# Kernel tuning notes

Measured on AMD Instinct MI355X. Metric: run time of the kernel, lower is better.

The kernel has to match this reference:

```python
import jax, jax.numpy as jnp
import numpy as np

T, B = 256, 256
IN_H, IN_T, IN_R = 64, 64, 32
H1, H2, H3 = 512, 1024, 256
H = H1 + H2 + H3
IN = IN_H + IN_T + IN_R
DT, TAU = 10.0, 30.0
ALPHA = DT / TAU
SIG1, SIG2, SIG3 = 0.1, 0.1, 0.1  # sigma_rec3 = sigma_rec1
RECUR1 = RECUR2 = FFWD = FBACK = 1.0


def _readin_mask():
    m = np.zeros((H, IN), dtype=np.float32)
    # row block 1 (h1): heading + targcolor
    m[:H1, :IN_H] = 1.0
    m[:H1, IN_H:IN_H + IN_T] = 1.0
    # row block 2 (h2): rules only
    m[H1:H1 + H2, IN_H + IN_T:] = 1.0
    # row block 3 (h3): targcolor only
    m[H1 + H2:, IN_H:IN_H + IN_T] = 1.0
    return jnp.asarray(m)


def _rec_mask():
    m = np.zeros((H, H), dtype=np.float32)
    m[:H1, :H1] = RECUR1
    m[:H1, H1:H1 + H2] = FBACK
    m[H1:H1 + H2, :H1] = FFWD
    m[H1:H1 + H2, H1:H1 + H2] = RECUR2
    m[H1:H1 + H2, H1 + H2:] = 1.0
    m[H1 + H2:, H1:H1 + H2] = 1.0
    m[H1 + H2:, H1 + H2:] = 1.0
    return jnp.asarray(m)


def _sigma_vec():
    # Faithful to source bug: segment 2 covers cols [H1:H2), leaving [H2:H1+H2) noiseless.
    s = np.zeros((H,), dtype=np.float32)
    s[:H1] = SIG1
    s[H1:H2] = SIG2
    s[H1 + H2:] = SIG3
    return jnp.asarray(s)


def setup_inputs() -> dict:
    key = jax.random.key(0)
    ks = jax.random.split(key, 5)
    bnd_in = 1.0 / np.sqrt(IN)
    bnd_rec = 1.0 / np.sqrt(H)
    return {
        "inputs": jax.random.normal(ks[0], (T, B, IN), dtype=jnp.float32),
        "W_in": jax.random.uniform(ks[1], (H, IN), minval=-bnd_in, maxval=bnd_in, dtype=jnp.float32),
        "b_in": jax.random.uniform(ks[2], (H,), minval=-bnd_in, maxval=bnd_in, dtype=jnp.float32),
        "W_rec": jax.random.uniform(ks[3], (H, H), minval=-bnd_rec, maxval=bnd_rec, dtype=jnp.float32),
        "b_rec": jax.random.uniform(ks[4], (H,), minval=-bnd_rec, maxval=bnd_rec, dtype=jnp.float32),
    }


def reference(inputs, W_in, b_in, W_rec, b_rec):
    mask_in = _readin_mask()
    mask_rec = _rec_mask()
    sigma = _sigma_vec()
    Weff_in = W_in * mask_in    # [H, IN]
    Weff_rec = W_rec * mask_rec  # [H, H]

    noise_keys = jax.random.split(jax.random.key(42), T)
    # precompute input projection for all steps: [T, B, H]
    xin = jnp.einsum('tbi,hi->tbh', inputs, Weff_in) + b_in

    def step(carry, xs):
        state, out = carry
        x_t, nk = xs
        total = x_t + out @ Weff_rec.T + b_rec  # [B, H]
        state = state * (1.0 - ALPHA) + total * ALPHA
        state = state + sigma * jax.random.normal(nk, state.shape, dtype=state.dtype)
        out = jax.nn.relu(state)
        return (state, out), out

    init = (jnp.zeros((B, H), dtype=inputs.dtype), jnp.zeros((B, H), dtype=inputs.dtype))
    (state, out), outputs = jax.lax.scan(step, init, (xin, noise_keys))
    return outputs, (state, out)
```

## Files before the change

kernel.cpp:

```cpp
#include <hip/hip_runtime.h>

#define T_STEPS 256
#define B_SZ 256
#define H_SZ 1792
#define IN_SZ 160
#define BH (B_SZ * H_SZ)
#define NSTEP_REC 56
#define NSTEP_X 5
#define NFRAG_H 112
#define APK_HALF (16 * NSTEP_REC * 2 * 512)
#define KS 8

typedef __attribute__((ext_vector_type(8))) _Float16 f16x8;
typedef __attribute__((ext_vector_type(4))) _Float16 f16x4;
typedef __attribute__((ext_vector_type(4))) float f32x4;

__device__ __forceinline__ unsigned rotl32(unsigned x, int r) {
  return (x << r) | (x >> (32 - r));
}

__device__ __forceinline__ void threefry2x32(unsigned k0, unsigned k1,
                                             unsigned x0, unsigned x1,
                                             unsigned& o0, unsigned& o1) {
  unsigned ks2 = k0 ^ k1 ^ 0x1BD11BDAu;
  x0 += k0; x1 += k1;
#define TF_R(r) { x0 += x1; x1 = rotl32(x1, (r)); x1 ^= x0; }
  TF_R(13) TF_R(15) TF_R(26) TF_R(6)
  x0 += k1; x1 += ks2 + 1u;
  TF_R(17) TF_R(29) TF_R(16) TF_R(24)
  x0 += ks2; x1 += k0 + 2u;
  TF_R(13) TF_R(15) TF_R(26) TF_R(6)
  x0 += k0; x1 += k1 + 3u;
  TF_R(17) TF_R(29) TF_R(16) TF_R(24)
  x0 += k1; x1 += ks2 + 4u;
  TF_R(13) TF_R(15) TF_R(26) TF_R(6)
  x0 += ks2; x1 += k0 + 5u;
#undef TF_R
  o0 = x0; o1 = x1;
}

__device__ __forceinline__ float erfinv_f32(float x) {
  float w = -log1pf(-x * x);
  float p;
  if (w < 5.0f) {
    w -= 2.5f;
    p = 2.81022636e-08f;
    p = fmaf(p, w, 3.43273939e-07f);
    p = fmaf(p, w, -3.5233877e-06f);
    p = fmaf(p, w, -4.39150654e-06f);
    p = fmaf(p, w, 0.00021858087f);
    p = fmaf(p, w, -0.00125372503f);
    p = fmaf(p, w, -0.00417768164f);
    p = fmaf(p, w, 0.246640727f);
    p = fmaf(p, w, 1.50140941f);
  } else {
    w = sqrtf(w) - 3.0f;
    p = -0.000200214257f;
    p = fmaf(p, w, 0.000100950558f);
    p = fmaf(p, w, 0.00134934322f);
    p = fmaf(p, w, -0.00367342844f);
    p = fmaf(p, w, 0.00573950773f);
    p = fmaf(p, w, -0.0076224613f);
    p = fmaf(p, w, 0.00943887047f);
    p = fmaf(p, w, 1.00167406f);
    p = fmaf(p, w, 2.83297682f);
  }
  return p * x;
}

__device__ __forceinline__ float jax_normal(unsigned k0, unsigned k1, unsigned e) {
  unsigned o0, o1;
  threefry2x32(k0, k1, 0u, e, o0, o1);
  const unsigned bits = o0 ^ o1;
  float u = __uint_as_float((bits >> 9) | 0x3F800000u) - 1.0f;
  float z = u * 2.0f + (-0.99999994f);
  z = fmaxf(-0.99999994f, z);
  return 1.4142135623730951f * erfinv_f32(z);
}

__global__ void init_keys_kernel(unsigned* __restrict__ keybuf) {
  const unsigned t = threadIdx.x;
  unsigned o0, o1;
  threefry2x32(0u, 42u, 0u, t, o0, o1);
  keybuf[2 * t] = o0;
  keybuf[2 * t + 1] = o1;
}

__device__ __forceinline__ void split2(float w, _Float16& h, _Float16& m) {
  h = (_Float16)w;
  float r = w - (float)h;
  m = (_Float16)(r * 2048.0f);
}

__global__ void pack_B_kernel(const float* __restrict__ W_in,
                              const float* __restrict__ W_rec,
                              _Float16* __restrict__ Bpk) {
  const int id = blockIdx.x * 256 + threadIdx.x;
  const int h = id / 244;
  const int ko = id - h * 244;
  const int k0 = ko * 8;
  float w[8];
  if (k0 < H_SZ) {
    const float4* src = reinterpret_cast<const float4*>(&W_rec[(size_t)h * H_SZ + k0]);
    float4 v0 = src[0], v1 = src[1];
    float m;
    if (h < 512)       m = (k0 < 1536) ? 1.0f : 0.0f;
    else if (h < 1536) m = 1.0f;
    else               m = (k0 >= 512) ? 1.0f : 0.0f;
    w[0]=v0.x*m; w[1]=v0.y*m; w[2]=v0.z*m; w[3]=v0.w*m;
    w[4]=v1.x*m; w[5]=v1.y*m; w[6]=v1.z*m; w[7]=v1.w*m;
  } else {
    const int i0 = k0 - H_SZ;
    const float4* src = reinterpret_cast<const float4*>(&W_in[(size_t)h * IN_SZ + i0]);
    float4 v0 = src[0], v1 = src[1];
    float m;
    if (h < 512)       m = (i0 < 128) ? 1.0f : 0.0f;
    else if (h < 1536) m = (i0 >= 128) ? 1.0f : 0.0f;
    else               m = (i0 >= 64 && i0 < 128) ? 1.0f : 0.0f;
    w[0]=v0.x*m; w[1]=v0.y*m; w[2]=v0.z*m; w[3]=v0.w*m;
    w[4]=v1.x*m; w[5]=v1.y*m; w[6]=v1.z*m; w[7]=v1.w*m;
  }
  f16x8 vh, vm;
#pragma unroll
  for (int j = 0; j < 8; ++j) {
    _Float16 a, b;
    split2(w[j], a, b);
    vh[j] = a; vm[j] = b;
  }
  const int s = ko >> 2;
  const int f = h >> 4;
  const int lane = (h & 15) + 16 * (ko & 3);
  _Float16* dst = Bpk + ((size_t)(s * NFRAG_H + f) * 2) * 512 + lane * 8;
  *reinterpret_cast<f16x8*>(dst)       = vh;
  *reinterpret_cast<f16x8*>(dst + 512) = vm;
}

__global__ void pack_x_kernel(const float* __restrict__ inputs,
                              _Float16* __restrict__ Xpk) {
  const int id = blockIdx.x * 256 + threadIdx.x;
  const int io = id % 20;
  const int tb = id / 20;
  const int b = tb & 255;
  const int t = tb >> 8;
  const float4* src = reinterpret_cast<const float4*>(
      &inputs[((size_t)(t * 256 + b)) * IN_SZ + io * 8]);
  float4 v0 = src[0], v1 = src[1];
  float w[8] = {v0.x, v0.y, v0.z, v0.w, v1.x, v1.y, v1.z, v1.w};
  f16x8 vh, vm;
#pragma unroll
  for (int j = 0; j < 8; ++j) {
    _Float16 a, bb;
    split2(w[j], a, bb);
    vh[j] = a; vm[j] = bb;
  }
  const int sx = io >> 2;
  const int lane = (b & 15) + 16 * (io & 3);
  _Float16* dst = Xpk +
      ((size_t)((t * 16 + (b >> 4)) * NSTEP_X + sx) * 2) * 512 + lane * 8;
  *reinterpret_cast<f16x8*>(dst)       = vh;
  *reinterpret_cast<f16x8*>(dst + 512) = vm;
}

__global__ void zero_kernel(float* __restrict__ p, int n) {
  const int i = blockIdx.x * 256 + threadIdx.x;
  if (i < n) p[i] = 0.0f;
}

__global__ __launch_bounds__(256) void xin_gemm(
    const _Float16* __restrict__ Xpk,
    const _Float16* __restrict__ Bpk,
    const float* __restrict__ b_in,
    float* __restrict__ out) {
  const int tid = threadIdx.x;
  const int w = tid >> 6;
  const int lane = tid & 63;
  const int t = blockIdx.x / 28;
  const int hb = blockIdx.x - t * 28;
  const int bf0 = w * 4;
  const int f0 = hb * 4;
  const int lofs = lane * 8;

  f32x4 acc1[4][4] = {};
  f32x4 acc2[4][4] = {};
#pragma unroll
  for (int s = 0; s < NSTEP_X; ++s) {
    f16x8 a[4][2], b[4][2];
#pragma unroll
    for (int pi = 0; pi < 4; ++pi) {
      const _Float16* ap = Xpk +
          ((size_t)((t * 16 + bf0 + pi) * NSTEP_X + s) * 2) * 512 + lofs;
      a[pi][0] = *reinterpret_cast<const f16x8*>(ap);
      a[pi][1] = *reinterpret_cast<const f16x8*>(ap + 512);
    }
#pragma unroll
    for (int qi = 0; qi < 4; ++qi) {
      const _Float16* bp = Bpk +
          ((size_t)(((NSTEP_REC + s) * NFRAG_H + f0 + qi) * 2)) * 512 + lofs;
      b[qi][0] = *reinterpret_cast<const f16x8*>(bp);
      b[qi][1] = *reinterpret_cast<const f16x8*>(bp + 512);
    }
#pragma unroll
    for (int pi = 0; pi < 4; ++pi)
#pragma unroll
      for (int qi = 0; qi < 4; ++qi) {
        acc1[pi][qi] = __builtin_amdgcn_mfma_f32_16x16x32_f16(
            a[pi][0], b[qi][0], acc1[pi][qi], 0, 0, 0);
        acc2[pi][qi] = __builtin_amdgcn_mfma_f32_16x16x32_f16(
            a[pi][0], b[qi][1], acc2[pi][qi], 0, 0, 0);
        acc2[pi][qi] = __builtin_amdgcn_mfma_f32_16x16x32_f16(
            a[pi][1], b[qi][0], acc2[pi][qi], 0, 0, 0);
      }
  }
#pragma unroll
  for (int qi = 0; qi < 4; ++qi) {
    const int h = hb * 64 + qi * 16 + (lane & 15);
    const float bi = b_in[h];
#pragma unroll
    for (int pi = 0; pi < 4; ++pi) {
      const int brow = (bf0 + pi) * 16 + ((lane >> 4) << 2);
#pragma unroll
      for (int r = 0; r < 4; ++r) {
        out[(size_t)t * BH + (size_t)(brow + r) * H_SZ + h] =
            acc1[pi][qi][r] + acc2[pi][qi][r] * (1.0f / 2048.0f) + bi;
      }
    }
  }
}

__global__ __launch_bounds__(512) void eirnn_step(
    const _Float16* __restrict__ Apk_cur,
    _Float16* __restrict__ Apk_next,
    const _Float16* __restrict__ Bpk,
    float* __restrict__ state,
    const float* __restrict__ b_rec,
    const unsigned* __restrict__ keybuf,
    float* __restrict__ out_t, int t) {
  __shared__ float ldsC[KS][32][68];

  const int tid = threadIdx.x;
  const int w = tid >> 6;
  const int lane = tid & 63;
  const int logical = (blockIdx.x & 7) * 28 + (blockIdx.x >> 3);
  const int hb = logical >> 3;
  const int bb = logical & 7;
  const int b0 = bb * 32;

  const int bf0 = b0 >> 4;
  const int f0 = hb * 4;
  const int lofs = lane * 8;

  int rec_lo, n;
  if (hb < 8)       { rec_lo = 0;  n = 48; }
  else if (hb < 24) { rec_lo = 0;  n = 56; }
  else              { rec_lo = 16; n = 40; }

  f32x4 acc1[2][4] = {};
  f32x4 acc2[2][4] = {};
  f16x8 bA[2][2][2];
  f16x8 bB[2][4][2];

#define LOAD(IB, I)                                                            \
  { const int s = rec_lo + (I);                                                \
    _Pragma("unroll")                                                          \
    for (int pi = 0; pi < 2; ++pi) {                                           \
      const _Float16* ap =                                                     \
          Apk_cur + ((size_t)((bf0 + pi) * NSTEP_REC + s) * 2) * 512 + lofs;   \
      bA[IB][pi][0] = *reinterpret_cast<const f16x8*>(ap);                     \
      bA[IB][pi][1] = *reinterpret_cast<const f16x8*>(ap + 512);               \
    }                                                                          \
    _Pragma("unroll")                                                          \
    for (int qi = 0; qi < 4; ++qi) {                                           \
      const _Float16* bp =                                                     \
          Bpk + ((size_t)(s * NFRAG_H + f0 + qi) * 2) * 512 + lofs;            \
      bB[IB][qi][0] = *reinterpret_cast<const f16x8*>(bp);                     \
      bB[IB][qi][1] = *reinterpret_cast<const f16x8*>(bp + 512);               \
    } }

#define MM(IB)                                                                 \
  { _Pragma("unroll")                                                          \
    for (int pi = 0; pi < 2; ++pi)                                             \
      _Pragma("unroll")                                                        \
      for (int qi = 0; qi < 4; ++qi) {                                         \
        acc1[pi][qi] = __builtin_amdgcn_mfma_f32_16x16x32_f16(                 \
            bA[IB][pi][0], bB[IB][qi][0], acc1[pi][qi], 0, 0, 0);              \
        acc2[pi][qi] = __builtin_amdgcn_mfma_f32_16x16x32_f16(                 \
            bA[IB][pi][0], bB[IB][qi][1], acc2[pi][qi], 0, 0, 0);              \
        acc2[pi][qi] = __builtin_amdgcn_mfma_f32_16x16x32_f16(                 \
            bA[IB][pi][1], bB[IB][qi][0], acc2[pi][qi], 0, 0, 0);              \
      } }

  LOAD(0, w)
  if (w + KS < n) LOAD(1, w + KS)

  const int bl = tid >> 4;
  const int q  = tid & 15;
  const int h0 = hb * 64 + q * 4;
  const size_t e0 = (size_t)(b0 + bl) * H_SZ + h0;
  const float sig = (h0 < 1024 || h0 >= 1536) ? 0.1f : 0.0f;
  float nz[4] = {0.0f, 0.0f, 0.0f, 0.0f};
  if (sig != 0.0f) {
    const unsigned kk0 = keybuf[2 * t], kk1 = keybuf[2 * t + 1];
#pragma unroll
    for (int j = 0; j < 4; ++j)
      nz[j] = jax_normal(kk0, kk1, (unsigned)(e0 + j));
  }
  const f32x4 xi = *reinterpret_cast<const f32x4*>(&out_t[e0]);
  const f32x4 sv = *reinterpret_cast<const f32x4*>(&state[e0]);
  const f32x4 br = *reinterpret_cast<const f32x4*>(&b_rec[h0]);

  for (int i = w; i < n; i += 2 * KS) {
    MM(0)
    if (i + 2 * KS < n) LOAD(0, i + 2 * KS)
    if (i + KS < n) {
      MM(1)
      if (i + 3 * KS < n) LOAD(1, i + 3 * KS)
    }
  }
#undef LOAD
#undef MM

#pragma unroll
  for (int pi = 0; pi < 2; ++pi)
#pragma unroll
    for (int qi = 0; qi < 4; ++qi) {
      const int row = pi * 16 + ((lane >> 4) << 2);
      const int col = qi * 16 + (lane & 15);
#pragma unroll
      for (int r = 0; r < 4; ++r)
        ldsC[w][row + r][col] =
            acc1[pi][qi][r] + acc2[pi][qi][r] * (1.0f / 2048.0f);
    }
  __syncthreads();

  f32x4 sum = {0.0f, 0.0f, 0.0f, 0.0f};
#pragma unroll
  for (int ww = 0; ww < KS; ++ww)
    sum += *reinterpret_cast<const f32x4*>(&ldsC[ww][bl][q * 4]);

  f32x4 so, oo;
  f16x4 vh, vm;
#pragma unroll
  for (int j = 0; j < 4; ++j) {
    float s = sv[j] * 0.6666666865348816f +
              (sum[j] + xi[j] + br[j]) * 0.3333333432674408f;
    s += sig * nz[j];
    const float o = fmaxf(s, 0.0f);
    so[j] = s; oo[j] = o;
    _Float16 xh, xm;
    split2(o, xh, xm);
    vh[j] = xh; vm[j] = xm;
  }
  *reinterpret_cast<f32x4*>(&state[e0]) = so;
  *reinterpret_cast<f32x4*>(&out_t[e0]) = oo;

  const int b = b0 + bl;
  _Float16* dst = Apk_next +
      ((size_t)((b >> 4) * NSTEP_REC + hb * 2 + (q >> 3)) * 2) * 512 +
      ((b & 15) + 16 * ((q >> 1) & 3)) * 8 + (q & 1) * 4;
  *reinterpret_cast<f16x4*>(dst)       = vh;
  *reinterpret_cast<f16x4*>(dst + 512) = vm;
}

__global__ void finalize_kernel(const float* __restrict__ state,
                                const float* __restrict__ last_out,
                                float* __restrict__ dst) {
  const int i = blockIdx.x * 256 + threadIdx.x;
  dst[i] = state[i];
  dst[BH + i] = last_out[i];
}

extern "C" void kernel_launch(void* const* d_in, const int* in_sizes, int n_in,
                              void* d_out, int out_size, void* d_ws, size_t ws_size,
                              hipStream_t stream) {
  const float* inputs = (const float*)d_in[0];
  const float* W_in   = (const float*)d_in[1];
  const float* b_in   = (const float*)d_in[2];
  const float* W_rec  = (const float*)d_in[3];
  const float* b_rec  = (const float*)d_in[4];
  float* out = (float*)d_out;

  char* ws = (char*)d_ws;
  _Float16* Bpk = (_Float16*)ws;
  _Float16* Xpk = (_Float16*)(ws + 13991936);
  _Float16* Apk = (_Float16*)(ws + 55934976);
  float* state  = (float*)(ws + 59604992);
  unsigned* keybuf = (unsigned*)(ws + 61440000);

  init_keys_kernel<<<1, 256, 0, stream>>>(keybuf);
  pack_B_kernel<<<1708, 256, 0, stream>>>(W_in, W_rec, Bpk);
  pack_x_kernel<<<5120, 256, 0, stream>>>(inputs, Xpk);
  zero_kernel<<<1792, 256, 0, stream>>>(state, BH);
  zero_kernel<<<1792, 256, 0, stream>>>((float*)Apk, APK_HALF / 2);

  xin_gemm<<<T_STEPS * 28, 256, 0, stream>>>(Xpk, Bpk, b_in, out);

  for (int t = 0; t < T_STEPS; ++t) {
    const int par = t & 1;
    eirnn_step<<<224, 512, 0, stream>>>(
        Apk + (size_t)par * APK_HALF,
        Apk + (size_t)(par ^ 1) * APK_HALF,
        Bpk, state, b_rec, keybuf, out + (size_t)t * BH, t);
  }

  finalize_kernel<<<1792, 256, 0, stream>>>(
      state, out + (size_t)(T_STEPS - 1) * BH, out + (size_t)T_STEPS * BH);
}
```

Baseline: 3.380 ms.

## Replace per-step RNN launches with persistent kernel and software grid barrier

Merges the 256 per-timestep launches into one persistent kernel of 224 blocks. The blocks synchronise through an atomic generation-counter grid barrier. State stays in registers across steps. The previous step's fp32 output is read directly from the output buffer and split into fp16 hi/lo in registers, which removes the packed Apk buffers, the zero kernels and the finalize kernel. This cuts launch overhead and some global traffic, in exchange for a spin barrier that relies on all blocks being co-resident, plus extra conversion work and wider fp32 A loads inside the MFMA loop.

Result: slower. 6.618 ms (+95.8%).

```diff
diff --git a/kernel.cpp b/kernel.cpp
--- a/kernel.cpp
+++ b/kernel.cpp
@@ -8,12 +8,14 @@
 #define NSTEP_REC 56
 #define NSTEP_X 5
 #define NFRAG_H 112
-#define APK_HALF (16 * NSTEP_REC * 2 * 512)
 #define KS 8
+#define NBLOCKS 224
 
 typedef __attribute__((ext_vector_type(8))) _Float16 f16x8;
-typedef __attribute__((ext_vector_type(4))) _Float16 f16x4;
 typedef __attribute__((ext_vector_type(4))) float f32x4;
+typedef unsigned long long u64;
+
+union U64F32x4 { u64 u[2]; f32x4 v; };
 
 __device__ __forceinline__ unsigned rotl32(unsigned x, int r) {
   return (x << r) | (x >> (32 - r));
@@ -78,12 +80,14 @@
   return 1.4142135623730951f * erfinv_f32(z);
 }
 
-__global__ void init_keys_kernel(unsigned* __restrict__ keybuf) {
+__global__ void init_keys_kernel(unsigned* __restrict__ keybuf,
+                                 unsigned* __restrict__ bar) {
   const unsigned t = threadIdx.x;
   unsigned o0, o1;
   threefry2x32(0u, 42u, 0u, t, o0, o1);
   keybuf[2 * t] = o0;
   keybuf[2 * t + 1] = o1;
+  if (t == 0) bar[0] = 0u;
 }
 
 __device__ __forceinline__ void split2(float w, _Float16& h, _Float16& m) {
@@ -161,11 +165,6 @@
   *reinterpret_cast<f16x8*>(dst + 512) = vm;
 }
 
-__global__ void zero_kernel(float* __restrict__ p, int n) {
-  const int i = blockIdx.x * 256 + threadIdx.x;
-  if (i < n) p[i] = 0.0f;
-}
-
 __global__ __launch_bounds__(256) void xin_gemm(
     const _Float16* __restrict__ Xpk,
     const _Float16* __restrict__ Bpk,
@@ -227,14 +226,33 @@
   }
 }
 
-__global__ __launch_bounds__(512) void eirnn_step(
-    const _Float16* __restrict__ Apk_cur,
-    _Float16* __restrict__ Apk_next,
+__device__ __forceinline__ void grid_barrier(unsigned* bar) {
+  __syncthreads();
+  if (threadIdx.x == 0) {
+    const unsigned gen = __hip_atomic_load(bar + 1, __ATOMIC_RELAXED,
+                                           __HIP_MEMORY_SCOPE_AGENT);
+    const unsigned pos = __hip_atomic_fetch_add(bar, 1u, __ATOMIC_RELAXED,
+                                                __HIP_MEMORY_SCOPE_AGENT);
+    if (pos == NBLOCKS - 1) {
+      __hip_atomic_store(bar, 0u, __ATOMIC_RELAXED, __HIP_MEMORY_SCOPE_AGENT);
+      __hip_atomic_store(bar + 1, gen + 1u, __ATOMIC_RELAXED,
+                         __HIP_MEMORY_SCOPE_AGENT);
+    } else {
+      while (__hip_atomic_load(bar + 1, __ATOMIC_RELAXED,
+                               __HIP_MEMORY_SCOPE_AGENT) == gen) {
+        __builtin_amdgcn_s_sleep(2);
+      }
+    }
+  }
+  asm volatile("" ::: "memory");
+  __syncthreads();
+}
+
+__global__ __launch_bounds__(512, 2) void eirnn_persist(
     const _Float16* __restrict__ Bpk,
-    float* __restrict__ state,
     const float* __restrict__ b_rec,
     const unsigned* __restrict__ keybuf,
-    float* __restrict__ out_t, int t) {
+    float* __restrict__ out, unsigned* __restrict__ bar) {
   __shared__ float ldsC[KS][32][68];
 
   const int tid = threadIdx.x;
@@ -245,7 +263,6 @@
   const int bb = logical & 7;
   const int b0 = bb * 32;
 
-  const int bf0 = b0 >> 4;
   const int f0 = hb * 4;
   const int lofs = lane * 8;
 
@@ -254,119 +271,143 @@
   else if (hb < 24) { rec_lo = 0;  n = 56; }
   else              { rec_lo = 16; n = 40; }
 
-  f32x4 acc1[2][4] = {};
-  f32x4 acc2[2][4] = {};
-  f16x8 bA[2][2][2];
-  f16x8 bB[2][4][2];
-
-#define LOAD(IB, I)                                                            \
-  { const int s = rec_lo + (I);                                                \
-    _Pragma("unroll")                                                          \
-    for (int pi = 0; pi < 2; ++pi) {                                           \
-      const _Float16* ap =                                                     \
-          Apk_cur + ((size_t)((bf0 + pi) * NSTEP_REC + s) * 2) * 512 + lofs;   \
-      bA[IB][pi][0] = *reinterpret_cast<const f16x8*>(ap);                     \
-      bA[IB][pi][1] = *reinterpret_cast<const f16x8*>(ap + 512);               \
-    }                                                                          \
-    _Pragma("unroll")                                                          \
-    for (int qi = 0; qi < 4; ++qi) {                                           \
-      const _Float16* bp =                                                     \
-          Bpk + ((size_t)(s * NFRAG_H + f0 + qi) * 2) * 512 + lofs;            \
-      bB[IB][qi][0] = *reinterpret_cast<const f16x8*>(bp);                     \
-      bB[IB][qi][1] = *reinterpret_cast<const f16x8*>(bp + 512);               \
-    } }
-
-#define MM(IB)                                                                 \
-  { _Pragma("unroll")                                                          \
-    for (int pi = 0; pi < 2; ++pi)                                             \
-      _Pragma("unroll")                                                        \
-      for (int qi = 0; qi < 4; ++qi) {                                         \
-        acc1[pi][qi] = __builtin_amdgcn_mfma_f32_16x16x32_f16(                 \
-            bA[IB][pi][0], bB[IB][qi][0], acc1[pi][qi], 0, 0, 0);              \
-        acc2[pi][qi] = __builtin_amdgcn_mfma_f32_16x16x32_f16(                 \
-            bA[IB][pi][0], bB[IB][qi][1], acc2[pi][qi], 0, 0, 0);              \
-        acc2[pi][qi] = __builtin_amdgcn_mfma_f32_16x16x32_f16(                 \
-            bA[IB][pi][1], bB[IB][qi][0], acc2[pi][qi], 0, 0, 0);              \
-      } }
-
-  LOAD(0, w)
-  if (w + KS < n) LOAD(1, w + KS)
+  const size_t rowbase0 =
+      (size_t)(b0 + (lane & 15)) * H_SZ + ((lane >> 4) << 3);
+  const size_t rowbase1 = rowbase0 + (size_t)16 * H_SZ;
 
   const int bl = tid >> 4;
   const int q  = tid & 15;
   const int h0 = hb * 64 + q * 4;
   const size_t e0 = (size_t)(b0 + bl) * H_SZ + h0;
   const float sig = (h0 < 1024 || h0 >= 1536) ? 0.1f : 0.0f;
-  float nz[4] = {0.0f, 0.0f, 0.0f, 0.0f};
-  if (sig != 0.0f) {
+  const f32x4 br = *reinterpret_cast<const f32x4*>(&b_rec[h0]);
+
+  f32x4 sv = {0.0f, 0.0f, 0.0f, 0.0f};
+
+#define COMPUTE_NZ_XI                                                          \
+  if (sig != 0.0f) {                                                           \
+    _Pragma("unroll")                                                          \
+    for (int j = 0; j < 4; ++j) nz[j] = jax_normal(kk0, kk1, (unsigned)(e0 + j)); \
+  }                                                                            \
+  { U64F32x4 xu;                                                               \
+    const u64* xp = (const u64*)(out + (size_t)t * BH + e0);                   \
+    xu.u[0] = __hip_atomic_load(xp, __ATOMIC_RELAXED, __HIP_MEMORY_SCOPE_AGENT); \
+    xu.u[1] = __hip_atomic_load(xp + 1, __ATOMIC_RELAXED, __HIP_MEMORY_SCOPE_AGENT); \
+    xi = xu.v; }
+
+  for (int t = 0; t < T_STEPS; ++t) {
     const unsigned kk0 = keybuf[2 * t], kk1 = keybuf[2 * t + 1];
-#pragma unroll
-    for (int j = 0; j < 4; ++j)
-      nz[j] = jax_normal(kk0, kk1, (unsigned)(e0 + j));
-  }
-  const f32x4 xi = *reinterpret_cast<const f32x4*>(&out_t[e0]);
-  const f32x4 sv = *reinterpret_cast<const f32x4*>(&state[e0]);
-  const f32x4 br = *reinterpret_cast<const f32x4*>(&b_rec[h0]);
-
-  for (int i = w; i < n; i += 2 * KS) {
-    MM(0)
-    if (i + 2 * KS < n) LOAD(0, i + 2 * KS)
-    if (i + KS < n) {
-      MM(1)
-      if (i + 3 * KS < n) LOAD(1, i + 3 * KS)
-    }
-  }
-#undef LOAD
+    float nz[4] = {0.0f, 0.0f, 0.0f, 0.0f};
+    f32x4 xi;
+    f32x4 sum = {0.0f, 0.0f, 0.0f, 0.0f};
+
+    if (t > 0) {
+      const float* outPrev = out + (size_t)(t - 1) * BH;
+      f32x4 acc1[2][4] = {};
+      f32x4 acc2[2][4] = {};
+      f32x4 rA[2][2][2];
+      f16x8 bB[2][4][2];
+
+#define LOADA(IB, I)                                                           \
+  { const int s_ = rec_lo + (I);                                               \
+    rA[IB][0][0] = *reinterpret_cast<const f32x4*>(outPrev + rowbase0 + 32 * s_);     \
+    rA[IB][0][1] = *reinterpret_cast<const f32x4*>(outPrev + rowbase0 + 32 * s_ + 4); \
+    rA[IB][1][0] = *reinterpret_cast<const f32x4*>(outPrev + rowbase1 + 32 * s_);     \
+    rA[IB][1][1] = *reinterpret_cast<const f32x4*>(outPrev + rowbase1 + 32 * s_ + 4); }
+#define LOADB(IB, I)                                                           \
+  { const int s_ = rec_lo + (I);                                               \
+    _Pragma("unroll")                                                          \
+    for (int qi = 0; qi < 4; ++qi) {                                           \
+      const _Float16* bp =                                                     \
+          Bpk + ((size_t)(s_ * NFRAG_H + f0 + qi) * 2) * 512 + lofs;           \
+      bB[IB][qi][0] = *reinterpret_cast<const f16x8*>(bp);                     \
+      bB[IB][qi][1] = *reinterpret_cast<const f16x8*>(bp + 512);               \
+    } }
+#define MM(IB)                                                                 \
+  { _Pragma("unroll")                                                          \
+    for (int pi = 0; pi < 2; ++pi) {                                           \
+      f16x8 ah, am;                                                            \
+      _Pragma("unroll")                                                        \
+      for (int c = 0; c < 2; ++c)                                              \
+        _Pragma("unroll")                                                      \
+        for (int j = 0; j < 4; ++j) {                                          \
+          const float v = rA[IB][pi][c][j];                                    \
+          const _Float16 hh = (_Float16)v;                                     \
+          const float r_ = v - (float)hh;                                      \
+          ah[c * 4 + j] = hh;                                                  \
+          am[c * 4 + j] = (_Float16)(r_ * 2048.0f);                            \
+        }                                                                      \
+      _Pragma("unroll")                                                        \
+      for (int qi = 0; qi < 4; ++qi) {                                         \
+        acc1[pi][qi] = __builtin_amdgcn_mfma_f32_16x16x32_f16(                 \
+            ah, bB[IB][qi][0], acc1[pi][qi], 0, 0, 0);                         \
+        acc2[pi][qi] = __builtin_amdgcn_mfma_f32_16x16x32_f16(                 \
+            ah, bB[IB][qi][1], acc2[pi][qi], 0, 0, 0);                         \
+        acc2[pi][qi] = __builtin_amdgcn_mfma_f32_16x16x32_f16(                 \
+            am, bB[IB][qi][0], acc2[pi][qi], 0, 0, 0);                         \
+      } } }
+
+      LOADA(0, w) LOADB(0, w)
+      if (w + KS < n) { LOADA(1, w + KS) LOADB(1, w + KS) }
+
+      COMPUTE_NZ_XI
+
+      for (int i = w; i < n; i += 2 * KS) {
+        MM(0)
+        if (i + 2 * KS < n) { LOADA(0, i + 2 * KS) LOADB(0, i + 2 * KS) }
+        if (i + KS < n) {
+          MM(1)
+          if (i + 3 * KS < n) { LOADA(1, i + 3 * KS) LOADB(1, i + 3 * KS) }
+        }
+      }
+#undef LOADA
+#undef LOADB
 #undef MM
 
 #pragma unroll
-  for (int pi = 0; pi < 2; ++pi)
-#pragma unroll
-    for (int qi = 0; qi < 4; ++qi) {
-      const int row = pi * 16 + ((lane >> 4) << 2);
-      const int col = qi * 16 + (lane & 15);
-#pragma unroll
-      for (int r = 0; r < 4; ++r)
-        ldsC[w][row + r][col] =
-            acc1[pi][qi][r] + acc2[pi][qi][r] * (1.0f / 2048.0f);
-    }
-  __syncthreads();
-
-  f32x4 sum = {0.0f, 0.0f, 0.0f, 0.0f};
-#pragma unroll
-  for (int ww = 0; ww < KS; ++ww)
-    sum += *reinterpret_cast<const f32x4*>(&ldsC[ww][bl][q * 4]);
-
-  f32x4 so, oo;
-  f16x4 vh, vm;
-#pragma unroll
-  for (int j = 0; j < 4; ++j) {
-    float s = sv[j] * 0.6666666865348816f +
-              (sum[j] + xi[j] + br[j]) * 0.3333333432674408f;
-    s += sig * nz[j];
-    const float o = fmaxf(s, 0.0f);
-    so[j] = s; oo[j] = o;
-    _Float16 xh, xm;
-    split2(o, xh, xm);
-    vh[j] = xh; vm[j] = xm;
-  }
-  *reinterpret_cast<f32x4*>(&state[e0]) = so;
-  *reinterpret_cast<f32x4*>(&out_t[e0]) = oo;
-
-  const int b = b0 + bl;
-  _Float16* dst = Apk_next +
-      ((size_t)((b >> 4) * NSTEP_REC + hb * 2 + (q >> 3)) * 2) * 512 +
-      ((b & 15) + 16 * ((q >> 1) & 3)) * 8 + (q & 1) * 4;
-  *reinterpret_cast<f16x4*>(dst)       = vh;
-  *reinterpret_cast<f16x4*>(dst + 512) = vm;
-}
-
-__global__ void finalize_kernel(const float* __restrict__ state,
-                                const float* __restrict__ last_out,
-                                float* __restrict__ dst) {
-  const int i = blockIdx.x * 256 + threadIdx.x;
-  dst[i] = state[i];
-  dst[BH + i] = last_out[i];
+      for (int pi = 0; pi < 2; ++pi)
+#pragma unroll
+        for (int qi = 0; qi < 4; ++qi) {
+          const int row = pi * 16 + ((lane >> 4) << 2);
+          const int col = qi * 16 + (lane & 15);
+#pragma unroll
+          for (int r = 0; r < 4; ++r)
+            ldsC[w][row + r][col] =
+                acc1[pi][qi][r] + acc2[pi][qi][r] * (1.0f / 2048.0f);
+        }
+      __syncthreads();
+
+#pragma unroll
+      for (int ww = 0; ww < KS; ++ww)
+        sum += *reinterpret_cast<const f32x4*>(&ldsC[ww][bl][q * 4]);
+    } else {
+      COMPUTE_NZ_XI
+    }
+
+    f32x4 so, oo;
+#pragma unroll
+    for (int j = 0; j < 4; ++j) {
+      float s = sv[j] * 0.6666666865348816f +
+                (sum[j] + xi[j] + br[j]) * 0.3333333432674408f;
+      s += sig * nz[j];
+      so[j] = s;
+      oo[j] = fmaxf(s, 0.0f);
+    }
+    sv = so;
+
+    if (t < T_STEPS - 1) {
+      U64F32x4 ou; ou.v = oo;
+      u64* op = (u64*)(out + (size_t)t * BH + e0);
+      __hip_atomic_store(op, ou.u[0], __ATOMIC_RELAXED, __HIP_MEMORY_SCOPE_AGENT);
+      __hip_atomic_store(op + 1, ou.u[1], __ATOMIC_RELAXED, __HIP_MEMORY_SCOPE_AGENT);
+      grid_barrier(bar);
+    } else {
+      *reinterpret_cast<f32x4*>(&out[(size_t)t * BH + e0]) = oo;
+      *reinterpret_cast<f32x4*>(&out[(size_t)T_STEPS * BH + e0]) = so;
+      *reinterpret_cast<f32x4*>(&out[(size_t)T_STEPS * BH + BH + e0]) = oo;
+    }
+  }
+#undef COMPUTE_NZ_XI
 }
 
 extern "C" void kernel_launch(void* const* d_in, const int* in_sizes, int n_in,
@@ -382,26 +423,14 @@
   char* ws = (char*)d_ws;
   _Float16* Bpk = (_Float16*)ws;
   _Float16* Xpk = (_Float16*)(ws + 13991936);
-  _Float16* Apk = (_Float16*)(ws + 55934976);
-  float* state  = (float*)(ws + 59604992);
-  unsigned* keybuf = (unsigned*)(ws + 61440000);
-
-  init_keys_kernel<<<1, 256, 0, stream>>>(keybuf);
+  unsigned* keybuf = (unsigned*)(ws + 55934976);
+  unsigned* bar = (unsigned*)(ws + 55937152);
+
+  init_keys_kernel<<<1, 256, 0, stream>>>(keybuf, bar);
   pack_B_kernel<<<1708, 256, 0, stream>>>(W_in, W_rec, Bpk);
   pack_x_kernel<<<5120, 256, 0, stream>>>(inputs, Xpk);
-  zero_kernel<<<1792, 256, 0, stream>>>(state, BH);
-  zero_kernel<<<1792, 256, 0, stream>>>((float*)Apk, APK_HALF / 2);
 
   xin_gemm<<<T_STEPS * 28, 256, 0, stream>>>(Xpk, Bpk, b_in, out);
 
-  for (int t = 0; t < T_STEPS; ++t) {
-    const int par = t & 1;
-    eirnn_step<<<224, 512, 0, stream>>>(
-        Apk + (size_t)par * APK_HALF,
-        Apk + (size_t)(par ^ 1) * APK_HALF,
-        Bpk, state, b_rec, keybuf, out + (size_t)t * BH, t);
-  }
-
-  finalize_kernel<<<1792, 256, 0, stream>>>(
-      state, out + (size_t)(T_STEPS - 1) * BH, out + (size_t)T_STEPS * BH);
-}
+  eirnn_persist<<<NBLOCKS, 512, 0, stream>>>(Bpk, b_rec, keybuf, out, bar);
+}
```

## Deepen recurrent step prefetch pipeline and skip zero-state first step

Applied to the files above, without the earlier changes.

The recurrent step kernel's K loop is fully unrolled into at most seven stages. A-fragments are now prefetched four stages ahead and B-fragments three ahead, replacing the old two-deep double buffer, so more global loads are in flight while MFMAs run. At t=0 the matmul is skipped because the previous output is zero, and the state is taken as zero. This removes the two zero-fill kernels for state and the packed activation buffer. It costs more registers per thread, which may lower occupancy or cause spills.

Result: slower. 4.344 ms (+28.5%).

```diff
diff --git a/kernel.cpp b/kernel.cpp
--- a/kernel.cpp
+++ b/kernel.cpp
@@ -161,11 +161,6 @@
   *reinterpret_cast<f16x8*>(dst + 512) = vm;
 }
 
-__global__ void zero_kernel(float* __restrict__ p, int n) {
-  const int i = blockIdx.x * 256 + threadIdx.x;
-  if (i < n) p[i] = 0.0f;
-}
-
 __global__ __launch_bounds__(256) void xin_gemm(
     const _Float16* __restrict__ Xpk,
     const _Float16* __restrict__ Bpk,
@@ -253,96 +248,114 @@
   if (hb < 8)       { rec_lo = 0;  n = 48; }
   else if (hb < 24) { rec_lo = 0;  n = 56; }
   else              { rec_lo = 16; n = 40; }
-
-  f32x4 acc1[2][4] = {};
-  f32x4 acc2[2][4] = {};
-  f16x8 bA[2][2][2];
-  f16x8 bB[2][4][2];
-
-#define LOAD(IB, I)                                                            \
-  { const int s = rec_lo + (I);                                                \
+  const int m = n >> 3;
+
+  const int bl = tid >> 4;
+  const int q  = tid & 15;
+  const int h0 = hb * 64 + q * 4;
+  const size_t e0 = (size_t)(b0 + bl) * H_SZ + h0;
+  const float sig = (h0 < 1024 || h0 >= 1536) ? 0.1f : 0.0f;
+
+  f32x4 sum = {0.0f, 0.0f, 0.0f, 0.0f};
+  float nz[4] = {0.0f, 0.0f, 0.0f, 0.0f};
+  f32x4 xi, sv, brv;
+
+  if (t > 0) {
+    f32x4 acc1[2][4] = {};
+    f32x4 acc2[2][4] = {};
+    f16x8 bA[4][2][2];
+    f16x8 bB[3][4][2];
+
+#define LOADA(IA, J)                                                           \
+  { const int s_ = rec_lo + w + 8 * (J);                                       \
     _Pragma("unroll")                                                          \
     for (int pi = 0; pi < 2; ++pi) {                                           \
       const _Float16* ap =                                                     \
-          Apk_cur + ((size_t)((bf0 + pi) * NSTEP_REC + s) * 2) * 512 + lofs;   \
-      bA[IB][pi][0] = *reinterpret_cast<const f16x8*>(ap);                     \
-      bA[IB][pi][1] = *reinterpret_cast<const f16x8*>(ap + 512);               \
-    }                                                                          \
+          Apk_cur + ((size_t)((bf0 + pi) * NSTEP_REC + s_) * 2) * 512 + lofs;  \
+      bA[IA][pi][0] = *reinterpret_cast<const f16x8*>(ap);                     \
+      bA[IA][pi][1] = *reinterpret_cast<const f16x8*>(ap + 512);               \
+    } }
+#define LOADB(IB, J)                                                           \
+  { const int s_ = rec_lo + w + 8 * (J);                                       \
     _Pragma("unroll")                                                          \
     for (int qi = 0; qi < 4; ++qi) {                                           \
       const _Float16* bp =                                                     \
-          Bpk + ((size_t)(s * NFRAG_H + f0 + qi) * 2) * 512 + lofs;            \
+          Bpk + ((size_t)(s_ * NFRAG_H + f0 + qi) * 2) * 512 + lofs;           \
       bB[IB][qi][0] = *reinterpret_cast<const f16x8*>(bp);                     \
       bB[IB][qi][1] = *reinterpret_cast<const f16x8*>(bp + 512);               \
     } }
-
-#define MM(IB)                                                                 \
+#define MM(IB, IA)                                                             \
   { _Pragma("unroll")                                                          \
     for (int pi = 0; pi < 2; ++pi)                                             \
       _Pragma("unroll")                                                        \
       for (int qi = 0; qi < 4; ++qi) {                                         \
         acc1[pi][qi] = __builtin_amdgcn_mfma_f32_16x16x32_f16(                 \
-            bA[IB][pi][0], bB[IB][qi][0], acc1[pi][qi], 0, 0, 0);              \
+            bA[IA][pi][0], bB[IB][qi][0], acc1[pi][qi], 0, 0, 0);              \
         acc2[pi][qi] = __builtin_amdgcn_mfma_f32_16x16x32_f16(                 \
-            bA[IB][pi][0], bB[IB][qi][1], acc2[pi][qi], 0, 0, 0);              \
+            bA[IA][pi][0], bB[IB][qi][1], acc2[pi][qi], 0, 0, 0);              \
         acc2[pi][qi] = __builtin_amdgcn_mfma_f32_16x16x32_f16(                 \
-            bA[IB][pi][1], bB[IB][qi][0], acc2[pi][qi], 0, 0, 0);              \
+            bA[IA][pi][1], bB[IB][qi][0], acc2[pi][qi], 0, 0, 0);              \
       } }
-
-  LOAD(0, w)
-  if (w + KS < n) LOAD(1, w + KS)
-
-  const int bl = tid >> 4;
-  const int q  = tid & 15;
-  const int h0 = hb * 64 + q * 4;
-  const size_t e0 = (size_t)(b0 + bl) * H_SZ + h0;
-  const float sig = (h0 < 1024 || h0 >= 1536) ? 0.1f : 0.0f;
-  float nz[4] = {0.0f, 0.0f, 0.0f, 0.0f};
-  if (sig != 0.0f) {
-    const unsigned kk0 = keybuf[2 * t], kk1 = keybuf[2 * t + 1];
-#pragma unroll
-    for (int j = 0; j < 4; ++j)
-      nz[j] = jax_normal(kk0, kk1, (unsigned)(e0 + j));
-  }
-  const f32x4 xi = *reinterpret_cast<const f32x4*>(&out_t[e0]);
-  const f32x4 sv = *reinterpret_cast<const f32x4*>(&state[e0]);
-  const f32x4 br = *reinterpret_cast<const f32x4*>(&b_rec[h0]);
-
-  for (int i = w; i < n; i += 2 * KS) {
-    MM(0)
-    if (i + 2 * KS < n) LOAD(0, i + 2 * KS)
-    if (i + KS < n) {
-      MM(1)
-      if (i + 3 * KS < n) LOAD(1, i + 3 * KS)
+#define STEP(J)                                                                \
+  if ((J) < m) {                                                               \
+    MM((J) % 3, (J) & 3)                                                       \
+    if ((J) + 3 < m) LOADB(((J) + 3) % 3, (J) + 3)                             \
+    if ((J) + 4 < m) LOADA(((J) + 4) & 3, (J) + 4)                             \
+  }
+
+    LOADA(0, 0) LOADA(1, 1) LOADA(2, 2) LOADA(3, 3)
+    LOADB(0, 0) LOADB(1, 1) LOADB(2, 2)
+
+    if (sig != 0.0f) {
+      const unsigned kk0 = keybuf[2 * t], kk1 = keybuf[2 * t + 1];
+#pragma unroll
+      for (int j = 0; j < 4; ++j)
+        nz[j] = jax_normal(kk0, kk1, (unsigned)(e0 + j));
     }
-  }
-#undef LOAD
+    xi = *reinterpret_cast<const f32x4*>(&out_t[e0]);
+    sv = *reinterpret_cast<const f32x4*>(&state[e0]);
+    brv = *reinterpret_cast<const f32x4*>(&b_rec[h0]);
+
+    STEP(0) STEP(1) STEP(2) STEP(3) STEP(4) STEP(5) STEP(6)
+#undef LOADA
+#undef LOADB
 #undef MM
-
-#pragma unroll
-  for (int pi = 0; pi < 2; ++pi)
-#pragma unroll
-    for (int qi = 0; qi < 4; ++qi) {
-      const int row = pi * 16 + ((lane >> 4) << 2);
-      const int col = qi * 16 + (lane & 15);
-#pragma unroll
-      for (int r = 0; r < 4; ++r)
-        ldsC[w][row + r][col] =
-            acc1[pi][qi][r] + acc2[pi][qi][r] * (1.0f / 2048.0f);
+#undef STEP
+
+#pragma unroll
+    for (int pi = 0; pi < 2; ++pi)
+#pragma unroll
+      for (int qi = 0; qi < 4; ++qi) {
+        const int row = pi * 16 + ((lane >> 4) << 2);
+        const int col = qi * 16 + (lane & 15);
+#pragma unroll
+        for (int r = 0; r < 4; ++r)
+          ldsC[w][row + r][col] =
+              acc1[pi][qi][r] + acc2[pi][qi][r] * (1.0f / 2048.0f);
+      }
+    __syncthreads();
+
+#pragma unroll
+    for (int ww = 0; ww < KS; ++ww)
+      sum += *reinterpret_cast<const f32x4*>(&ldsC[ww][bl][q * 4]);
+  } else {
+    if (sig != 0.0f) {
+      const unsigned kk0 = keybuf[0], kk1 = keybuf[1];
+#pragma unroll
+      for (int j = 0; j < 4; ++j)
+        nz[j] = jax_normal(kk0, kk1, (unsigned)(e0 + j));
     }
-  __syncthreads();
-
-  f32x4 sum = {0.0f, 0.0f, 0.0f, 0.0f};
-#pragma unroll
-  for (int ww = 0; ww < KS; ++ww)
-    sum += *reinterpret_cast<const f32x4*>(&ldsC[ww][bl][q * 4]);
+    xi = *reinterpret_cast<const f32x4*>(&out_t[e0]);
+    sv = (f32x4){0.0f, 0.0f, 0.0f, 0.0f};
+    brv = *reinterpret_cast<const f32x4*>(&b_rec[h0]);
+  }
 
   f32x4 so, oo;
   f16x4 vh, vm;
 #pragma unroll
   for (int j = 0; j < 4; ++j) {
     float s = sv[j] * 0.6666666865348816f +
-              (sum[j] + xi[j] + br[j]) * 0.3333333432674408f;
+              (sum[j] + xi[j] + brv[j]) * 0.3333333432674408f;
     s += sig * nz[j];
     const float o = fmaxf(s, 0.0f);
     so[j] = s; oo[j] = o;
@@ -389,8 +402,6 @@
   init_keys_kernel<<<1, 256, 0, stream>>>(keybuf);
   pack_B_kernel<<<1708, 256, 0, stream>>>(W_in, W_rec, Bpk);
   pack_x_kernel<<<5120, 256, 0, stream>>>(inputs, Xpk);
-  zero_kernel<<<1792, 256, 0, stream>>>(state, BH);
-  zero_kernel<<<1792, 256, 0, stream>>>((float*)Apk, APK_HALF / 2);
 
   xin_gemm<<<T_STEPS * 28, 256, 0, stream>>>(Xpk, Bpk, b_in, out);
 
```
